# Performance work log

Hardware: AMD Instinct MI355X
Metric: run time of the kernel (lower is better)

The kernel has to match this reference:

```python
import jax, jax.numpy as jnp
import numpy as np

EPS = 1e-08  # attention offset, matches module epsilon


def _ln(x, g, b, eps=1e-5):
    m = jnp.mean(x, axis=-1, keepdims=True)
    v = jnp.var(x, axis=-1, keepdims=True)
    return (x - m) * jax.lax.rsqrt(v + eps) * g + b


def setup_inputs() -> dict:
    key = jax.random.key(0)
    ks = jax.random.split(key, 12)
    B, N, D, S, H = 32, 16384, 64, 7, 128
    sc = 1.0 / np.sqrt(D)
    sch = 1.0 / np.sqrt(H)
    return {
        "inputs": jax.random.normal(ks[0], (B, N, D), jnp.float32),
        "ln_in_g": jnp.ones((D,), jnp.float32), "ln_in_b": jnp.zeros((D,), jnp.float32),
        "ln_slots_g": jnp.ones((D,), jnp.float32), "ln_slots_b": jnp.zeros((D,), jnp.float32),
        "ln_mlp_g": jnp.ones((D,), jnp.float32), "ln_mlp_b": jnp.zeros((D,), jnp.float32),
        "Wq": jax.random.normal(ks[1], (D, D), jnp.float32) * sc,
        "Wk": jax.random.normal(ks[2], (D, D), jnp.float32) * sc,
        "Wv": jax.random.normal(ks[3], (D, D), jnp.float32) * sc,
        "slots_mu": jax.random.normal(ks[4], (1, 1, D), jnp.float32),
        "slots_log_sigma": jax.random.normal(ks[5], (1, 1, D), jnp.float32) * 0.1,
        "w_ih": jax.random.normal(ks[6], (3 * D, D), jnp.float32) * sc,
        "w_hh": jax.random.normal(ks[7], (3 * D, D), jnp.float32) * sc,
        "b_ih": jnp.zeros((3 * D,), jnp.float32), "b_hh": jnp.zeros((3 * D,), jnp.float32),
        "mlp_w1": jax.random.normal(ks[8], (H, D), jnp.float32) * sc,
        "mlp_b1": jnp.zeros((H,), jnp.float32),
        "mlp_w2": jax.random.normal(ks[9], (D, H), jnp.float32) * sch,
        "mlp_b2": jnp.zeros((D,), jnp.float32),
        "noise_slots": jax.random.normal(ks[10], (B, S, D), jnp.float32),
        "noise_h": jax.random.normal(ks[11], (B, D), jnp.float32),
        "num_iterations": 3,
    }


def reference(inputs, ln_in_g, ln_in_b, ln_slots_g, ln_slots_b, ln_mlp_g, ln_mlp_b,
              Wq, Wk, Wv, slots_mu, slots_log_sigma, w_ih, w_hh, b_ih, b_hh,
              mlp_w1, mlp_b1, mlp_w2, mlp_b2, noise_slots, noise_h, num_iterations):
    D = inputs.shape[-1]
    scale = D ** -0.5

    x = _ln(inputs, ln_in_g, ln_in_b)               # [B,N,D]
    k = jnp.einsum('bnd,ed->bne', x, Wk)            # [B,N,D]
    v = jnp.einsum('bnd,ed->bne', x, Wv)            # [B,N,D]

    sigma = jnp.exp(slots_log_sigma)
    slots = slots_mu + sigma * noise_slots          # [B,S,D]
    h0 = (slots_mu + sigma * noise_h[None])[0]      # [B,D] (torch h0 is [1,B,D])

    def gru_step(h, x_t):  # torch GRU cell, gate order r,z,n
        gi = x_t @ w_ih.T + b_ih
        gh = h @ w_hh.T + b_hh
        ir, iz, inn = jnp.split(gi, 3, axis=-1)
        hr, hz, hn = jnp.split(gh, 3, axis=-1)
        r = jax.nn.sigmoid(ir + hr)
        z = jax.nn.sigmoid(iz + hz)
        n = jnp.tanh(inn + r * hn)
        h_new = (1.0 - z) * n + z * h
        return h_new, h_new

    for _ in range(num_iterations):
        sn = _ln(slots, ln_slots_g, ln_slots_b)
        q = jnp.einsum('bsd,ed->bse', sn, Wq) * scale        # [B,S,D]
        logits = jnp.einsum('bnd,bsd->bns', k, q)            # [B,N,S]
        attn = jax.nn.softmax(logits, axis=-1) + EPS          # softmax over slots
        attn = attn / jnp.sum(attn, axis=1, keepdims=True)   # normalize over inputs (dim=-2)
        updates = jnp.einsum('bns,bnd->bsd', attn, v)        # [B,S,D]
        # nn.GRU over the slot axis as "time", fixed h0 each iteration
        _, hs = jax.lax.scan(gru_step, h0, jnp.swapaxes(updates, 0, 1))
        slots = jnp.swapaxes(hs, 0, 1)                       # [B,S,D]
        hid = jax.nn.relu(_ln(slots, ln_mlp_g, ln_mlp_b) @ mlp_w1.T + mlp_b1)
        slots = slots + (hid @ mlp_w2.T + mlp_b2)
    return slots
```

## Files before the change

kernel.cpp:

```cpp
#include <hip/hip_runtime.h>
#include <hip/hip_bf16.h>


#define B_ 32
#define N_ 16384
#define D_ 64
#define S_ 7

typedef __bf16 bf16x8 __attribute__((ext_vector_type(8)));
typedef float floatx4 __attribute__((ext_vector_type(4)));

__device__ __forceinline__ unsigned int f2bfu(float f) {
  __hip_bfloat16 h = __float2bfloat16(f);
  return (unsigned int)__builtin_bit_cast(unsigned short, h);
}
__device__ __forceinline__ unsigned int pack2bf(float lo, float hi) {
  return f2bfu(lo) | (f2bfu(hi) << 16);
}

__global__ __launch_bounds__(256) void proj_kernel(
    const float* __restrict__ x,
    const float* __restrict__ lng, const float* __restrict__ lnb,
    const float* __restrict__ Wk, const float* __restrict__ Wv,
    unsigned short* __restrict__ kt, unsigned short* __restrict__ vb)
{
  __shared__ __align__(16) unsigned short s_xn[128 * 64];
  __shared__ __align__(16) unsigned short s_w[128 * 64];
  const int t = threadIdx.x;
  const int lane = t & 63;
  const int w = t >> 6;
  const int R0 = blockIdx.x * 128;
  const int bb = R0 >> 14;
  const int nbase = R0 & (N_ - 1);

  for (int j = 0; j < 2; ++j) {
    int idx = (t + j * 256) * 16;
    const float* src = (idx < 4096) ? (Wk + idx) : (Wv + idx - 4096);
    float4 a = ((const float4*)src)[0], b = ((const float4*)src)[1];
    float4 c = ((const float4*)src)[2], d = ((const float4*)src)[3];
    uint4 p0, p1;
    p0.x = pack2bf(a.x, a.y); p0.y = pack2bf(a.z, a.w);
    p0.z = pack2bf(b.x, b.y); p0.w = pack2bf(b.z, b.w);
    p1.x = pack2bf(c.x, c.y); p1.y = pack2bf(c.z, c.w);
    p1.z = pack2bf(d.x, d.y); p1.w = pack2bf(d.z, d.w);
    ((uint4*)s_w)[idx >> 3] = p0;
    ((uint4*)s_w)[(idx >> 3) + 1] = p1;
  }

  const int ql = t & 3;
  float4 g4[4], b4[4];
#pragma unroll
  for (int j = 0; j < 4; ++j) {
    g4[j] = *(const float4*)&lng[ql * 16 + j * 4];
    b4[j] = *(const float4*)&lnb[ql * 16 + j * 4];
  }
#pragma unroll
  for (int half = 0; half < 2; ++half) {
    int r = half * 64 + (t >> 2);
    const float4* xp = (const float4*)&x[(size_t)(R0 + r) * 64 + ql * 16];
    float4 xv[4];
#pragma unroll
    for (int j = 0; j < 4; ++j) xv[j] = xp[j];
    float s1 = 0.f, s2 = 0.f;
#pragma unroll
    for (int j = 0; j < 4; ++j) {
      s1 += xv[j].x + xv[j].y + xv[j].z + xv[j].w;
      s2 += xv[j].x * xv[j].x + xv[j].y * xv[j].y + xv[j].z * xv[j].z + xv[j].w * xv[j].w;
    }
    s1 += __shfl_xor(s1, 1); s2 += __shfl_xor(s2, 1);
    s1 += __shfl_xor(s1, 2); s2 += __shfl_xor(s2, 2);
    float mean = s1 * 0.015625f;
    float var = s2 * 0.015625f - mean * mean;
    float rs = rsqrtf(var + 1e-5f);
    float y[16];
#pragma unroll
    for (int j = 0; j < 4; ++j) {
      y[j * 4 + 0] = (xv[j].x - mean) * rs * g4[j].x + b4[j].x;
      y[j * 4 + 1] = (xv[j].y - mean) * rs * g4[j].y + b4[j].y;
      y[j * 4 + 2] = (xv[j].z - mean) * rs * g4[j].z + b4[j].z;
      y[j * 4 + 3] = (xv[j].w - mean) * rs * g4[j].w + b4[j].w;
    }
#pragma unroll
    for (int h = 0; h < 2; ++h) {
      uint4 p;
      p.x = pack2bf(y[h * 8 + 0], y[h * 8 + 1]);
      p.y = pack2bf(y[h * 8 + 2], y[h * 8 + 3]);
      p.z = pack2bf(y[h * 8 + 4], y[h * 8 + 5]);
      p.w = pack2bf(y[h * 8 + 6], y[h * 8 + 7]);
      int c = ql * 2 + h;
      int sc = c ^ (r & 7);
      *(uint4*)&s_xn[r * 64 + sc * 8] = p;
    }
  }
  __syncthreads();

  const int m16 = lane & 15, quad = lane >> 4;
  bf16x8 bf[2][2];
#pragma unroll
  for (int rt = 0; rt < 2; ++rt) {
    int xr = (w * 2 + rt) * 16 + m16;
#pragma unroll
    for (int kt2 = 0; kt2 < 2; ++kt2)
      bf[rt][kt2] = *(const bf16x8*)&s_xn[xr * 64 + (((kt2 * 4 + quad) ^ (xr & 7)) * 8)];
  }

#pragma unroll
  for (int ft = 0; ft < 4; ++ft) {
    bf16x8 wk0 = *(const bf16x8*)&s_w[(ft * 16 + m16) * 64 + quad * 8];
    bf16x8 wk1 = *(const bf16x8*)&s_w[(ft * 16 + m16) * 64 + 32 + quad * 8];
#pragma unroll
    for (int rt = 0; rt < 2; ++rt) {
      floatx4 acc = (floatx4){0.f, 0.f, 0.f, 0.f};
      acc = __builtin_amdgcn_mfma_f32_16x16x32_bf16(bf[rt][0], wk0, acc, 0, 0, 0);
      acc = __builtin_amdgcn_mfma_f32_16x16x32_bf16(bf[rt][1], wk1, acc, 0, 0, 0);
      int n_l = nbase + (w * 2 + rt) * 16 + quad * 4;
      size_t off = ((size_t)bb * 64 + ft * 16 + m16) * N_ + n_l;
      uint2 p;
      p.x = pack2bf(acc[0], acc[1]);
      p.y = pack2bf(acc[2], acc[3]);
      *(uint2*)&kt[off] = p;
    }
  }

#pragma unroll
  for (int mt = 0; mt < 4; ++mt) {
    bf16x8 wv0 = *(const bf16x8*)&s_w[(64 + mt * 16 + m16) * 64 + quad * 8];
    bf16x8 wv1 = *(const bf16x8*)&s_w[(64 + mt * 16 + m16) * 64 + 32 + quad * 8];
#pragma unroll
    for (int nt = 0; nt < 2; ++nt) {
      floatx4 acc = (floatx4){0.f, 0.f, 0.f, 0.f};
      acc = __builtin_amdgcn_mfma_f32_16x16x32_bf16(wv0, bf[nt][0], acc, 0, 0, 0);
      acc = __builtin_amdgcn_mfma_f32_16x16x32_bf16(wv1, bf[nt][1], acc, 0, 0, 0);
      int xrow_g = R0 + (w * 2 + nt) * 16 + m16;
      int col = mt * 16 + quad * 4;
      uint2 p;
      p.x = pack2bf(acc[0], acc[1]);
      p.y = pack2bf(acc[2], acc[3]);
      *(uint2*)&vb[(size_t)xrow_g * 64 + col] = p;
    }
  }
}

__device__ void q_from_slots(const float* s_slot, float* s_tmp,
                             const float* __restrict__ g, const float* __restrict__ bb,
                             const float* __restrict__ Wq, float* __restrict__ qout,
                             int lane, int w)
{
  for (int ss = 0; ss < 2; ++ss) {
    int srow = ss * 4 + w;
    if (srow < 7) {
      float xv = s_slot[srow * 64 + lane];
      float s1 = xv, s2 = xv * xv;
#pragma unroll
      for (int mm = 1; mm < 64; mm <<= 1) {
        s1 += __shfl_xor(s1, mm);
        s2 += __shfl_xor(s2, mm);
      }
      float mean = s1 * 0.015625f;
      float var = s2 * 0.015625f - mean * mean;
      float rs = rsqrtf(var + 1e-5f);
      s_tmp[w * 64 + lane] = (xv - mean) * rs * g[lane] + bb[lane];
    }
    __syncthreads();
    if (srow < 7) {
      float acc = 0.f;
      const float* wr = Wq + lane * 64;
      const float* xr = s_tmp + w * 64;
      for (int d = 0; d < 64; ++d) acc += xr[d] * wr[d];
      qout[srow * 64 + lane] = acc * 0.125f;
    }
    __syncthreads();
  }
}

__global__ __launch_bounds__(256) void init_kernel(
    const float* __restrict__ mu, const float* __restrict__ lsig,
    const float* __restrict__ nslots, const float* __restrict__ nh,
    const float* __restrict__ ln_s_g, const float* __restrict__ ln_s_b,
    const float* __restrict__ Wq,
    float* __restrict__ qbuf, float* __restrict__ Wacc, float* __restrict__ Cacc,
    float* __restrict__ h0b)
{
  __shared__ float s_slot[448];
  __shared__ float s_tmp[256];
  const int b = blockIdx.x, t = threadIdx.x, lane = t & 63, w = t >> 6;
  for (int o = t; o < 448; o += 256) {
    int d = o & 63;
    s_slot[o] = mu[d] + expf(lsig[d]) * nslots[b * 448 + o];
    Wacc[b * 448 + o] = 0.f;
  }
  if (t < 64) h0b[b * 64 + t] = mu[t] + expf(lsig[t]) * nh[b * 64 + t];
  if (t < 8) Cacc[b * 8 + t] = 0.f;
  __syncthreads();
  q_from_slots(s_slot, s_tmp, ln_s_g, ln_s_b, Wq, qbuf + b * 448, lane, w);
}

__global__ __launch_bounds__(256) void attn_kernel(
    const unsigned short* __restrict__ kt, const unsigned short* __restrict__ vb,
    const float* __restrict__ qbuf,
    float* __restrict__ Wacc, float* __restrict__ Cacc)
{
  __shared__ __align__(16) float s_qt[64 * 8];
  __shared__ __align__(16) float s_attn[4][7 * 132];
  __shared__ __align__(16) float s_red[4][448];
  __shared__ float s_cred[4][8];

  const int b = blockIdx.y;
  const int t = threadIdx.x, lane = t & 63, w = t >> 6;

  for (int i = t; i < 448; i += 256) {
    int s = i >> 6, d = i & 63;
    s_qt[d * 8 + s] = qbuf[b * 448 + i];
  }
  if (t < 64) s_qt[t * 8 + 7] = 0.f;
  __syncthreads();

  const int n0 = blockIdx.x * 512 + w * 128;

  float lg[2][7];
#pragma unroll
  for (int j = 0; j < 2; ++j)
#pragma unroll
    for (int s = 0; s < 7; ++s) lg[j][s] = 0.f;

  const unsigned short* ktb = kt + (size_t)b * 64 * N_ + n0 + 2 * lane;
#pragma unroll 16
  for (int d = 0; d < 64; ++d) {
    unsigned int kk = *(const unsigned int*)(ktb + (size_t)d * N_);
    float k0 = __uint_as_float(kk << 16);
    float k1 = __uint_as_float(kk & 0xffff0000u);
    float4 qa = *(const float4*)&s_qt[d * 8];
    float4 qb = *(const float4*)&s_qt[d * 8 + 4];
    lg[0][0] += k0 * qa.x; lg[0][1] += k0 * qa.y; lg[0][2] += k0 * qa.z; lg[0][3] += k0 * qa.w;
    lg[0][4] += k0 * qb.x; lg[0][5] += k0 * qb.y; lg[0][6] += k0 * qb.z;
    lg[1][0] += k1 * qa.x; lg[1][1] += k1 * qa.y; lg[1][2] += k1 * qa.z; lg[1][3] += k1 * qa.w;
    lg[1][4] += k1 * qb.x; lg[1][5] += k1 * qb.y; lg[1][6] += k1 * qb.z;
  }

  float cloc[7];
#pragma unroll
  for (int s = 0; s < 7; ++s) cloc[s] = 0.f;
  float at[2][7];
#pragma unroll
  for (int j = 0; j < 2; ++j) {
    float mx = lg[j][0];
#pragma unroll
    for (int s = 1; s < 7; ++s) mx = fmaxf(mx, lg[j][s]);
    float sum = 0.f;
#pragma unroll
    for (int s = 0; s < 7; ++s) { at[j][s] = __expf(lg[j][s] - mx); sum += at[j][s]; }
    float inv = 1.f / sum;
#pragma unroll
    for (int s = 0; s < 7; ++s) { at[j][s] = at[j][s] * inv + 1e-8f; }
  }
#pragma unroll
  for (int s = 0; s < 7; ++s) {
    cloc[s] = at[0][s] + at[1][s];
    float2 p = {at[0][s], at[1][s]};
    *(float2*)&s_attn[w][s * 132 + 2 * lane] = p;
  }
  asm volatile("s_waitcnt lgkmcnt(0)" ::: "memory");

  const int rq = lane & 3, dq = lane >> 4 ? (lane >> 2) : (lane >> 2);
  float accs[7][4];
#pragma unroll
  for (int s = 0; s < 7; ++s)
#pragma unroll
    for (int j = 0; j < 4; ++j) accs[s][j] = 0.f;

  const unsigned short* vbb = vb + ((size_t)b * N_ + n0) * 64 + (size_t)dq * 4;
#pragma unroll 8
  for (int rr = 0; rr < 32; ++rr) {
    int r = rr * 4 + rq;
    uint2 vv = *(const uint2*)(vbb + (size_t)r * 64);
    float vf0 = __uint_as_float(vv.x << 16);
    float vf1 = __uint_as_float(vv.x & 0xffff0000u);
    float vf2 = __uint_as_float(vv.y << 16);
    float vf3 = __uint_as_float(vv.y & 0xffff0000u);
#pragma unroll
    for (int s = 0; s < 7; ++s) {
      float av = s_attn[w][s * 132 + r];
      accs[s][0] += av * vf0;
      accs[s][1] += av * vf1;
      accs[s][2] += av * vf2;
      accs[s][3] += av * vf3;
    }
  }
#pragma unroll
  for (int s = 0; s < 7; ++s)
#pragma unroll
    for (int j = 0; j < 4; ++j) {
      float v = accs[s][j];
      v += __shfl_xor(v, 1);
      v += __shfl_xor(v, 2);
      accs[s][j] = v;
    }
  if (rq == 0) {
#pragma unroll
    for (int s = 0; s < 7; ++s)
#pragma unroll
      for (int j = 0; j < 4; ++j)
        s_red[w][s * 64 + dq * 4 + j] = accs[s][j];
  }
#pragma unroll
  for (int s = 0; s < 7; ++s) {
    float c = cloc[s];
#pragma unroll
    for (int mm = 1; mm < 64; mm <<= 1) c += __shfl_xor(c, mm);
    cloc[s] = c;
  }
  if (lane == 0) {
#pragma unroll
    for (int s = 0; s < 7; ++s) s_cred[w][s] = cloc[s];
  }
  __syncthreads();
  if (w == 0) {
#pragma unroll
    for (int s = 0; s < 7; ++s) {
      float v = s_red[0][s * 64 + lane] + s_red[1][s * 64 + lane] +
                s_red[2][s * 64 + lane] + s_red[3][s * 64 + lane];
      atomicAdd(&Wacc[b * 448 + s * 64 + lane], v);
    }
    if (lane < 7) {
      float c = s_cred[0][lane] + s_cred[1][lane] + s_cred[2][lane] + s_cred[3][lane];
      atomicAdd(&Cacc[b * 8 + lane], c);
    }
  }
}

__global__ __launch_bounds__(256) void slot_update_kernel(
    float* __restrict__ Wacc, float* __restrict__ Cacc,
    const float* __restrict__ h0b,
    const float* __restrict__ w_ih, const float* __restrict__ w_hh,
    const float* __restrict__ b_ih, const float* __restrict__ b_hh,
    const float* __restrict__ ln_m_g, const float* __restrict__ ln_m_b,
    const float* __restrict__ w1, const float* __restrict__ b1,
    const float* __restrict__ w2, const float* __restrict__ b2,
    const float* __restrict__ ln_s_g, const float* __restrict__ ln_s_b,
    const float* __restrict__ Wq,
    float* __restrict__ qbuf, float* __restrict__ out)
{
  const int b = blockIdx.x, t = threadIdx.x, lane = t & 63, w = t >> 6;
  __shared__ float s_upd[448];
  __shared__ float s_gi[1344];
  __shared__ float s_h[64];
  __shared__ float s_gh[192];
  __shared__ float s_slot[448];
  __shared__ float s_tmp[256];

  for (int o = t; o < 448; o += 256) {
    int s = o >> 6;
    s_upd[o] = Wacc[b * 448 + o] / Cacc[b * 8 + s];
  }
  __syncthreads();
  for (int o = t; o < 1344; o += 256) {
    int s = o / 192, j = o - s * 192;
    float acc = b_ih[j];
    const float* wr = w_ih + j * 64;
    const float* ur = s_upd + s * 64;
    for (int d = 0; d < 64; ++d) acc += ur[d] * wr[d];
    s_gi[o] = acc;
  }
  if (t < 64) s_h[t] = h0b[b * 64 + t];
  __syncthreads();
  for (int s = 0; s < 7; ++s) {
    if (t < 192) {
      float acc = b_hh[t];
      const float* wr = w_hh + t * 64;
      for (int d = 0; d < 64; ++d) acc += s_h[d] * wr[d];
      s_gh[t] = acc;
    }
    __syncthreads();
    if (t < 64) {
      float ir = s_gi[s * 192 + t], iz = s_gi[s * 192 + 64 + t], inn = s_gi[s * 192 + 128 + t];
      float hr = s_gh[t], hz = s_gh[64 + t], hn = s_gh[128 + t];
      float r = 1.f / (1.f + expf(-(ir + hr)));
      float z = 1.f / (1.f + expf(-(iz + hz)));
      float n = tanhf(inn + r * hn);
      float hnew = (1.f - z) * n + z * s_h[t];
      s_slot[s * 64 + t] = hnew;
      s_h[t] = hnew;
    }
    __syncthreads();
  }
  float* s_sn = s_gi;
  float* s_hid = s_gi + 448;
  for (int ss = 0; ss < 2; ++ss) {
    int srow = ss * 4 + w;
    if (srow < 7) {
      float xv = s_slot[srow * 64 + lane];
      float s1 = xv, s2 = xv * xv;
#pragma unroll
      for (int mm = 1; mm < 64; mm <<= 1) {
        s1 += __shfl_xor(s1, mm);
        s2 += __shfl_xor(s2, mm);
      }
      float mean = s1 * 0.015625f;
      float var = s2 * 0.015625f - mean * mean;
      float rs = rsqrtf(var + 1e-5f);
      s_sn[srow * 64 + lane] = (xv - mean) * rs * ln_m_g[lane] + ln_m_b[lane];
    }
  }
  __syncthreads();
  for (int o = t; o < 896; o += 256) {
    int s = o >> 7, hh = o & 127;
    float acc = b1[hh];
    const float* wr = w1 + hh * 64;
    const float* xr = s_sn + s * 64;
    for (int d = 0; d < 64; ++d) acc += xr[d] * wr[d];
    s_hid[o] = fmaxf(acc, 0.f);
  }
  __syncthreads();
  for (int o = t; o < 448; o += 256) {
    int s = o >> 6, d = o & 63;
    float acc = b2[d];
    const float* wr = w2 + d * 128;
    const float* hr = s_hid + s * 128;
    for (int h = 0; h < 128; ++h) acc += hr[h] * wr[h];
    float val = s_slot[o] + acc;
    s_slot[o] = val;
    out[b * 448 + o] = val;
  }
  for (int o = t; o < 448; o += 256) Wacc[b * 448 + o] = 0.f;
  if (t < 8) Cacc[b * 8 + t] = 0.f;
  __syncthreads();
  q_from_slots(s_slot, s_tmp, ln_s_g, ln_s_b, Wq, qbuf + b * 448, lane, w);
}

extern "C" void kernel_launch(void* const* d_in, const int* in_sizes, int n_in,
                              void* d_out, int out_size, void* d_ws, size_t ws_size,
                              hipStream_t stream)
{
  (void)in_sizes; (void)n_in; (void)out_size; (void)ws_size;
  const float* x      = (const float*)d_in[0];
  const float* ln_in_g = (const float*)d_in[1];
  const float* ln_in_b = (const float*)d_in[2];
  const float* ln_s_g  = (const float*)d_in[3];
  const float* ln_s_b  = (const float*)d_in[4];
  const float* ln_m_g  = (const float*)d_in[5];
  const float* ln_m_b  = (const float*)d_in[6];
  const float* Wq = (const float*)d_in[7];
  const float* Wk = (const float*)d_in[8];
  const float* Wv = (const float*)d_in[9];
  const float* mu = (const float*)d_in[10];
  const float* lsig = (const float*)d_in[11];
  const float* w_ih = (const float*)d_in[12];
  const float* w_hh = (const float*)d_in[13];
  const float* b_ih = (const float*)d_in[14];
  const float* b_hh = (const float*)d_in[15];
  const float* w1 = (const float*)d_in[16];
  const float* b1 = (const float*)d_in[17];
  const float* w2 = (const float*)d_in[18];
  const float* b2 = (const float*)d_in[19];
  const float* nslots = (const float*)d_in[20];
  const float* nh = (const float*)d_in[21];

  unsigned short* kt = (unsigned short*)d_ws;
  unsigned short* vb = kt + (size_t)B_ * N_ * D_;
  float* fb = (float*)(vb + (size_t)B_ * N_ * D_);
  float* qbuf = fb;
  float* Wacc = fb + 14336;
  float* Cacc = fb + 28672;
  float* h0b  = fb + 28928;
  float* out = (float*)d_out;

  proj_kernel<<<4096, 256, 0, stream>>>(x, ln_in_g, ln_in_b, Wk, Wv, kt, vb);
  init_kernel<<<32, 256, 0, stream>>>(mu, lsig, nslots, nh, ln_s_g, ln_s_b, Wq,
                                      qbuf, Wacc, Cacc, h0b);
  for (int it = 0; it < 3; ++it) {
    attn_kernel<<<dim3(32, 32), 256, 0, stream>>>(kt, vb, qbuf, Wacc, Cacc);
    slot_update_kernel<<<32, 256, 0, stream>>>(Wacc, Cacc, h0b, w_ih, w_hh, b_ih, b_hh,
                                               ln_m_g, ln_m_b, w1, b1, w2, b2,
                                               ln_s_g, ln_s_b, Wq, qbuf, out);
  }
}
```

Measured before the change: 488.8 us.

## Use MFMA for attention logits and updates with row-major K and transposed V

Swaps the storage layouts: K is now written row-major [B,N,D] and V transposed [B,D,N], each staged through LDS so global stores are coalesced. The attention kernel then computes logits and the attention-weighted V sum with bf16 MFMA instead of scalar FMA loops, doing the slot softmax with lane shuffles. Attention weights are rounded to bf16, which costs some precision. The slot update kernel stages w_hh transposed in LDS for the GRU recurrence, and several small dot products use float4 loads.

After: 423.5 us. -13.4%, faster.

```diff
diff --git a/kernel.cpp b/kernel.cpp
--- a/kernel.cpp
+++ b/kernel.cpp
@@ -22,29 +22,28 @@
     const float* __restrict__ x,
     const float* __restrict__ lng, const float* __restrict__ lnb,
     const float* __restrict__ Wk, const float* __restrict__ Wv,
-    unsigned short* __restrict__ kt, unsigned short* __restrict__ vb)
-{
-  __shared__ __align__(16) unsigned short s_xn[128 * 64];
-  __shared__ __align__(16) unsigned short s_w[128 * 64];
-  const int t = threadIdx.x;
-  const int lane = t & 63;
-  const int w = t >> 6;
+    unsigned short* __restrict__ kb, unsigned short* __restrict__ vt)
+{
+  __shared__ __align__(16) unsigned char smem[32768];
+  unsigned short* s_xn = (unsigned short*)smem;
+  unsigned short* s_w  = (unsigned short*)(smem + 16384);
+  unsigned short* s_ko = (unsigned short*)smem;
+  unsigned short* s_vo = (unsigned short*)smem;
+
+  const int t = threadIdx.x, lane = t & 63, w = t >> 6;
   const int R0 = blockIdx.x * 128;
   const int bb = R0 >> 14;
   const int nbase = R0 & (N_ - 1);
 
-  for (int j = 0; j < 2; ++j) {
-    int idx = (t + j * 256) * 16;
+#pragma unroll
+  for (int p = 0; p < 4; ++p) {
+    int idx = (p * 256 + t) * 8;
     const float* src = (idx < 4096) ? (Wk + idx) : (Wv + idx - 4096);
     float4 a = ((const float4*)src)[0], b = ((const float4*)src)[1];
-    float4 c = ((const float4*)src)[2], d = ((const float4*)src)[3];
-    uint4 p0, p1;
-    p0.x = pack2bf(a.x, a.y); p0.y = pack2bf(a.z, a.w);
-    p0.z = pack2bf(b.x, b.y); p0.w = pack2bf(b.z, b.w);
-    p1.x = pack2bf(c.x, c.y); p1.y = pack2bf(c.z, c.w);
-    p1.z = pack2bf(d.x, d.y); p1.w = pack2bf(d.z, d.w);
-    ((uint4*)s_w)[idx >> 3] = p0;
-    ((uint4*)s_w)[(idx >> 3) + 1] = p1;
+    uint4 pk;
+    pk.x = pack2bf(a.x, a.y); pk.y = pack2bf(a.z, a.w);
+    pk.z = pack2bf(b.x, b.y); pk.w = pack2bf(b.z, b.w);
+    *(uint4*)&s_w[idx] = pk;
   }
 
   const int ql = t & 3;
@@ -100,44 +99,63 @@
   for (int rt = 0; rt < 2; ++rt) {
     int xr = (w * 2 + rt) * 16 + m16;
 #pragma unroll
-    for (int kt2 = 0; kt2 < 2; ++kt2)
-      bf[rt][kt2] = *(const bf16x8*)&s_xn[xr * 64 + (((kt2 * 4 + quad) ^ (xr & 7)) * 8)];
-  }
-
-#pragma unroll
-  for (int ft = 0; ft < 4; ++ft) {
-    bf16x8 wk0 = *(const bf16x8*)&s_w[(ft * 16 + m16) * 64 + quad * 8];
-    bf16x8 wk1 = *(const bf16x8*)&s_w[(ft * 16 + m16) * 64 + 32 + quad * 8];
+    for (int kk = 0; kk < 2; ++kk)
+      bf[rt][kk] = *(const bf16x8*)&s_xn[xr * 64 + (((kk * 4 + quad) ^ (xr & 7)) * 8)];
+  }
+  bf16x8 wkf[4][2], wvf[4][2];
+#pragma unroll
+  for (int ft = 0; ft < 4; ++ft)
+#pragma unroll
+    for (int kk = 0; kk < 2; ++kk) {
+      wkf[ft][kk] = *(const bf16x8*)&s_w[(ft * 16 + m16) * 64 + kk * 32 + quad * 8];
+      wvf[ft][kk] = *(const bf16x8*)&s_w[(64 + ft * 16 + m16) * 64 + kk * 32 + quad * 8];
+    }
+  __syncthreads();
+
+#pragma unroll
+  for (int ft = 0; ft < 4; ++ft)
 #pragma unroll
     for (int rt = 0; rt < 2; ++rt) {
       floatx4 acc = (floatx4){0.f, 0.f, 0.f, 0.f};
-      acc = __builtin_amdgcn_mfma_f32_16x16x32_bf16(bf[rt][0], wk0, acc, 0, 0, 0);
-      acc = __builtin_amdgcn_mfma_f32_16x16x32_bf16(bf[rt][1], wk1, acc, 0, 0, 0);
-      int n_l = nbase + (w * 2 + rt) * 16 + quad * 4;
-      size_t off = ((size_t)bb * 64 + ft * 16 + m16) * N_ + n_l;
+      acc = __builtin_amdgcn_mfma_f32_16x16x32_bf16(wkf[ft][0], bf[rt][0], acc, 0, 0, 0);
+      acc = __builtin_amdgcn_mfma_f32_16x16x32_bf16(wkf[ft][1], bf[rt][1], acc, 0, 0, 0);
+      int n_l = (w * 2 + rt) * 16 + m16;
       uint2 p;
       p.x = pack2bf(acc[0], acc[1]);
       p.y = pack2bf(acc[2], acc[3]);
-      *(uint2*)&kt[off] = p;
-    }
-  }
-
-#pragma unroll
-  for (int mt = 0; mt < 4; ++mt) {
-    bf16x8 wv0 = *(const bf16x8*)&s_w[(64 + mt * 16 + m16) * 64 + quad * 8];
-    bf16x8 wv1 = *(const bf16x8*)&s_w[(64 + mt * 16 + m16) * 64 + 32 + quad * 8];
-#pragma unroll
-    for (int nt = 0; nt < 2; ++nt) {
+      *(uint2*)&s_ko[n_l * 72 + ft * 16 + quad * 4] = p;
+    }
+  __syncthreads();
+#pragma unroll
+  for (int p = 0; p < 4; ++p) {
+    int ii = (p * 256 + t) * 8;
+    int n_l = ii >> 6, dl = ii & 63;
+    uint4 v4 = *(const uint4*)&s_ko[n_l * 72 + dl];
+    *(uint4*)&kb[(size_t)(R0 + n_l) * 64 + dl] = v4;
+  }
+  __syncthreads();
+
+#pragma unroll
+  for (int ft = 0; ft < 4; ++ft)
+#pragma unroll
+    for (int rt = 0; rt < 2; ++rt) {
       floatx4 acc = (floatx4){0.f, 0.f, 0.f, 0.f};
-      acc = __builtin_amdgcn_mfma_f32_16x16x32_bf16(wv0, bf[nt][0], acc, 0, 0, 0);
-      acc = __builtin_amdgcn_mfma_f32_16x16x32_bf16(wv1, bf[nt][1], acc, 0, 0, 0);
-      int xrow_g = R0 + (w * 2 + nt) * 16 + m16;
-      int col = mt * 16 + quad * 4;
+      acc = __builtin_amdgcn_mfma_f32_16x16x32_bf16(bf[rt][0], wvf[ft][0], acc, 0, 0, 0);
+      acc = __builtin_amdgcn_mfma_f32_16x16x32_bf16(bf[rt][1], wvf[ft][1], acc, 0, 0, 0);
+      int n_l = (w * 2 + rt) * 16 + quad * 4;
+      int d0 = ft * 16 + m16;
       uint2 p;
       p.x = pack2bf(acc[0], acc[1]);
       p.y = pack2bf(acc[2], acc[3]);
-      *(uint2*)&vb[(size_t)xrow_g * 64 + col] = p;
-    }
+      *(uint2*)&s_vo[d0 * 136 + n_l] = p;
+    }
+  __syncthreads();
+#pragma unroll
+  for (int p = 0; p < 4; ++p) {
+    int ii = (p * 256 + t) * 8;
+    int d0 = ii >> 7, nl = ii & 127;
+    uint4 v4 = *(const uint4*)&s_vo[d0 * 136 + nl];
+    *(uint4*)&vt[((size_t)bb * 64 + d0) * N_ + nbase + nl] = v4;
   }
 }
 
@@ -164,9 +182,13 @@
     __syncthreads();
     if (srow < 7) {
       float acc = 0.f;
-      const float* wr = Wq + lane * 64;
-      const float* xr = s_tmp + w * 64;
-      for (int d = 0; d < 64; ++d) acc += xr[d] * wr[d];
+      const float4* wr = (const float4*)(Wq + lane * 64);
+      const float4* xr = (const float4*)(s_tmp + w * 64);
+#pragma unroll
+      for (int i = 0; i < 16; ++i) {
+        float4 a = wr[i], xx = xr[i];
+        acc += a.x * xx.x + a.y * xx.y + a.z * xx.z + a.w * xx.w;
+      }
       qout[srow * 64 + lane] = acc * 0.125f;
     }
     __syncthreads();
@@ -196,123 +218,99 @@
 }
 
 __global__ __launch_bounds__(256) void attn_kernel(
-    const unsigned short* __restrict__ kt, const unsigned short* __restrict__ vb,
+    const unsigned short* __restrict__ kb, const unsigned short* __restrict__ vt,
     const float* __restrict__ qbuf,
     float* __restrict__ Wacc, float* __restrict__ Cacc)
 {
-  __shared__ __align__(16) float s_qt[64 * 8];
-  __shared__ __align__(16) float s_attn[4][7 * 132];
+  __shared__ __align__(16) unsigned short s_qb[16 * 64];
+  __shared__ __align__(16) unsigned short s_at[4][16 * 136];
   __shared__ __align__(16) float s_red[4][448];
   __shared__ float s_cred[4][8];
 
   const int b = blockIdx.y;
   const int t = threadIdx.x, lane = t & 63, w = t >> 6;
-
-  for (int i = t; i < 448; i += 256) {
-    int s = i >> 6, d = i & 63;
-    s_qt[d * 8 + s] = qbuf[b * 448 + i];
-  }
-  if (t < 64) s_qt[t * 8 + 7] = 0.f;
-  __syncthreads();
-
-  const int n0 = blockIdx.x * 512 + w * 128;
-
-  float lg[2][7];
-#pragma unroll
-  for (int j = 0; j < 2; ++j)
-#pragma unroll
-    for (int s = 0; s < 7; ++s) lg[j][s] = 0.f;
-
-  const unsigned short* ktb = kt + (size_t)b * 64 * N_ + n0 + 2 * lane;
-#pragma unroll 16
-  for (int d = 0; d < 64; ++d) {
-    unsigned int kk = *(const unsigned int*)(ktb + (size_t)d * N_);
-    float k0 = __uint_as_float(kk << 16);
-    float k1 = __uint_as_float(kk & 0xffff0000u);
-    float4 qa = *(const float4*)&s_qt[d * 8];
-    float4 qb = *(const float4*)&s_qt[d * 8 + 4];
-    lg[0][0] += k0 * qa.x; lg[0][1] += k0 * qa.y; lg[0][2] += k0 * qa.z; lg[0][3] += k0 * qa.w;
-    lg[0][4] += k0 * qb.x; lg[0][5] += k0 * qb.y; lg[0][6] += k0 * qb.z;
-    lg[1][0] += k1 * qa.x; lg[1][1] += k1 * qa.y; lg[1][2] += k1 * qa.z; lg[1][3] += k1 * qa.w;
-    lg[1][4] += k1 * qb.x; lg[1][5] += k1 * qb.y; lg[1][6] += k1 * qb.z;
-  }
-
-  float cloc[7];
-#pragma unroll
-  for (int s = 0; s < 7; ++s) cloc[s] = 0.f;
-  float at[2][7];
-#pragma unroll
-  for (int j = 0; j < 2; ++j) {
-    float mx = lg[j][0];
-#pragma unroll
-    for (int s = 1; s < 7; ++s) mx = fmaxf(mx, lg[j][s]);
-    float sum = 0.f;
-#pragma unroll
-    for (int s = 0; s < 7; ++s) { at[j][s] = __expf(lg[j][s] - mx); sum += at[j][s]; }
-    float inv = 1.f / sum;
-#pragma unroll
-    for (int s = 0; s < 7; ++s) { at[j][s] = at[j][s] * inv + 1e-8f; }
-  }
-#pragma unroll
-  for (int s = 0; s < 7; ++s) {
-    cloc[s] = at[0][s] + at[1][s];
-    float2 p = {at[0][s], at[1][s]};
-    *(float2*)&s_attn[w][s * 132 + 2 * lane] = p;
+  const int m16 = lane & 15, quad = lane >> 4;
+
+  {
+    int i0 = t * 4;
+    int s = i0 >> 6, d0 = i0 & 63;
+    float f0 = 0.f, f1 = 0.f, f2 = 0.f, f3 = 0.f;
+    if (s < 7) {
+      const float* qp = qbuf + b * 448 + s * 64 + d0;
+      f0 = qp[0]; f1 = qp[1]; f2 = qp[2]; f3 = qp[3];
+    }
+    uint2 p;
+    p.x = pack2bf(f0, f1);
+    p.y = pack2bf(f2, f3);
+    *(uint2*)&s_qb[i0] = p;
+  }
+  __syncthreads();
+
+  bf16x8 bq0 = *(const bf16x8*)&s_qb[m16 * 64 + quad * 8];
+  bf16x8 bq1 = *(const bf16x8*)&s_qb[m16 * 64 + 32 + quad * 8];
+
+  const int n0w = blockIdx.x * 512 + w * 128;
+  const unsigned short* kbA = kb + ((size_t)b * N_ + n0w) * 64;
+
+  float cl = 0.f;
+#pragma unroll
+  for (int nt = 0; nt < 8; ++nt) {
+    bf16x8 a0 = *(const bf16x8*)&kbA[(size_t)(nt * 16 + m16) * 64 + quad * 8];
+    bf16x8 a1 = *(const bf16x8*)&kbA[(size_t)(nt * 16 + m16) * 64 + 32 + quad * 8];
+    floatx4 c = (floatx4){0.f, 0.f, 0.f, 0.f};
+    c = __builtin_amdgcn_mfma_f32_16x16x32_bf16(a0, bq0, c, 0, 0, 0);
+    c = __builtin_amdgcn_mfma_f32_16x16x32_bf16(a1, bq1, c, 0, 0, 0);
+    float atv[4];
+#pragma unroll
+    for (int rg = 0; rg < 4; ++rg) {
+      float xx = (m16 < 7) ? c[rg] : -1e30f;
+      float mx = xx;
+      mx = fmaxf(mx, __shfl_xor(mx, 1));
+      mx = fmaxf(mx, __shfl_xor(mx, 2));
+      mx = fmaxf(mx, __shfl_xor(mx, 4));
+      float e = __expf(xx - mx);
+      float sm = e;
+      sm += __shfl_xor(sm, 1);
+      sm += __shfl_xor(sm, 2);
+      sm += __shfl_xor(sm, 4);
+      float a = e / sm + 1e-8f;
+      atv[rg] = a;
+      cl += a;
+    }
+    if (m16 < 7) {
+      uint2 p;
+      p.x = pack2bf(atv[0], atv[1]);
+      p.y = pack2bf(atv[2], atv[3]);
+      *(uint2*)&s_at[w][m16 * 136 + nt * 16 + quad * 4] = p;
+    }
   }
   asm volatile("s_waitcnt lgkmcnt(0)" ::: "memory");
 
-  const int rq = lane & 3, dq = lane >> 4 ? (lane >> 2) : (lane >> 2);
-  float accs[7][4];
-#pragma unroll
-  for (int s = 0; s < 7; ++s)
-#pragma unroll
-    for (int j = 0; j < 4; ++j) accs[s][j] = 0.f;
-
-  const unsigned short* vbb = vb + ((size_t)b * N_ + n0) * 64 + (size_t)dq * 4;
-#pragma unroll 8
-  for (int rr = 0; rr < 32; ++rr) {
-    int r = rr * 4 + rq;
-    uint2 vv = *(const uint2*)(vbb + (size_t)r * 64);
-    float vf0 = __uint_as_float(vv.x << 16);
-    float vf1 = __uint_as_float(vv.x & 0xffff0000u);
-    float vf2 = __uint_as_float(vv.y << 16);
-    float vf3 = __uint_as_float(vv.y & 0xffff0000u);
-#pragma unroll
-    for (int s = 0; s < 7; ++s) {
-      float av = s_attn[w][s * 132 + r];
-      accs[s][0] += av * vf0;
-      accs[s][1] += av * vf1;
-      accs[s][2] += av * vf2;
-      accs[s][3] += av * vf3;
-    }
-  }
-#pragma unroll
-  for (int s = 0; s < 7; ++s)
-#pragma unroll
-    for (int j = 0; j < 4; ++j) {
-      float v = accs[s][j];
-      v += __shfl_xor(v, 1);
-      v += __shfl_xor(v, 2);
-      accs[s][j] = v;
-    }
-  if (rq == 0) {
-#pragma unroll
-    for (int s = 0; s < 7; ++s)
-#pragma unroll
-      for (int j = 0; j < 4; ++j)
-        s_red[w][s * 64 + dq * 4 + j] = accs[s][j];
-  }
-#pragma unroll
-  for (int s = 0; s < 7; ++s) {
-    float c = cloc[s];
-#pragma unroll
-    for (int mm = 1; mm < 64; mm <<= 1) c += __shfl_xor(c, mm);
-    cloc[s] = c;
-  }
-  if (lane == 0) {
-#pragma unroll
-    for (int s = 0; s < 7; ++s) s_cred[w][s] = cloc[s];
-  }
+  floatx4 acc[4];
+#pragma unroll
+  for (int dt = 0; dt < 4; ++dt) acc[dt] = (floatx4){0.f, 0.f, 0.f, 0.f};
+  const unsigned short* vtB = vt + (size_t)b * 64 * N_ + n0w;
+#pragma unroll
+  for (int ch = 0; ch < 4; ++ch) {
+    bf16x8 af = *(const bf16x8*)&s_at[w][m16 * 136 + ch * 32 + quad * 8];
+#pragma unroll
+    for (int dt = 0; dt < 4; ++dt) {
+      bf16x8 bv = *(const bf16x8*)&vtB[(size_t)(dt * 16 + m16) * N_ + ch * 32 + quad * 8];
+      acc[dt] = __builtin_amdgcn_mfma_f32_16x16x32_bf16(af, bv, acc[dt], 0, 0, 0);
+    }
+  }
+  if (quad < 2) {
+#pragma unroll
+    for (int dt = 0; dt < 4; ++dt)
+#pragma unroll
+      for (int rg = 0; rg < 4; ++rg) {
+        int s = quad * 4 + rg;
+        if (s < 7) s_red[w][s * 64 + dt * 16 + m16] = acc[dt][rg];
+      }
+  }
+  cl += __shfl_xor(cl, 16);
+  cl += __shfl_xor(cl, 32);
+  if (m16 < 7 && quad == 0) s_cred[w][m16] = cl;
   __syncthreads();
   if (w == 0) {
 #pragma unroll
@@ -341,6 +339,7 @@
     float* __restrict__ qbuf, float* __restrict__ out)
 {
   const int b = blockIdx.x, t = threadIdx.x, lane = t & 63, w = t >> 6;
+  __shared__ float s_whhT[64 * 201];
   __shared__ float s_upd[448];
   __shared__ float s_gi[1344];
   __shared__ float s_h[64];
@@ -348,26 +347,34 @@
   __shared__ float s_slot[448];
   __shared__ float s_tmp[256];
 
+  for (int i = t; i < 12288; i += 256) {
+    int j = i >> 6, d = i & 63;
+    s_whhT[d * 201 + j] = w_hh[i];
+  }
   for (int o = t; o < 448; o += 256) {
     int s = o >> 6;
     s_upd[o] = Wacc[b * 448 + o] / Cacc[b * 8 + s];
   }
+  if (t < 64) s_h[t] = h0b[b * 64 + t];
   __syncthreads();
   for (int o = t; o < 1344; o += 256) {
     int s = o / 192, j = o - s * 192;
     float acc = b_ih[j];
-    const float* wr = w_ih + j * 64;
-    const float* ur = s_upd + s * 64;
-    for (int d = 0; d < 64; ++d) acc += ur[d] * wr[d];
+    const float4* wr = (const float4*)(w_ih + j * 64);
+    const float4* ur = (const float4*)(s_upd + s * 64);
+#pragma unroll
+    for (int i = 0; i < 16; ++i) {
+      float4 a = wr[i], u = ur[i];
+      acc += a.x * u.x + a.y * u.y + a.z * u.z + a.w * u.w;
+    }
     s_gi[o] = acc;
   }
-  if (t < 64) s_h[t] = h0b[b * 64 + t];
   __syncthreads();
   for (int s = 0; s < 7; ++s) {
     if (t < 192) {
       float acc = b_hh[t];
-      const float* wr = w_hh + t * 64;
-      for (int d = 0; d < 64; ++d) acc += s_h[d] * wr[d];
+#pragma unroll 16
+      for (int d = 0; d < 64; ++d) acc += s_h[d] * s_whhT[d * 201 + t];
       s_gh[t] = acc;
     }
     __syncthreads();
@@ -405,18 +412,26 @@
   for (int o = t; o < 896; o += 256) {
     int s = o >> 7, hh = o & 127;
     float acc = b1[hh];
-    const float* wr = w1 + hh * 64;
-    const float* xr = s_sn + s * 64;
-    for (int d = 0; d < 64; ++d) acc += xr[d] * wr[d];
+    const float4* wr = (const float4*)(w1 + hh * 64);
+    const float4* xr = (const float4*)(s_sn + s * 64);
+#pragma unroll
+    for (int i = 0; i < 16; ++i) {
+      float4 a = wr[i], xx = xr[i];
+      acc += a.x * xx.x + a.y * xx.y + a.z * xx.z + a.w * xx.w;
+    }
     s_hid[o] = fmaxf(acc, 0.f);
   }
   __syncthreads();
   for (int o = t; o < 448; o += 256) {
     int s = o >> 6, d = o & 63;
     float acc = b2[d];
-    const float* wr = w2 + d * 128;
-    const float* hr = s_hid + s * 128;
-    for (int h = 0; h < 128; ++h) acc += hr[h] * wr[h];
+    const float4* wr = (const float4*)(w2 + d * 128);
+    const float4* hr = (const float4*)(s_hid + s * 128);
+#pragma unroll
+    for (int i = 0; i < 32; ++i) {
+      float4 a = wr[i], hv = hr[i];
+      acc += a.x * hv.x + a.y * hv.y + a.z * hv.z + a.w * hv.w;
+    }
     float val = s_slot[o] + acc;
     s_slot[o] = val;
     out[b * 448 + o] = val;
@@ -455,20 +470,20 @@
   const float* nslots = (const float*)d_in[20];
   const float* nh = (const float*)d_in[21];
 
-  unsigned short* kt = (unsigned short*)d_ws;
-  unsigned short* vb = kt + (size_t)B_ * N_ * D_;
-  float* fb = (float*)(vb + (size_t)B_ * N_ * D_);
+  unsigned short* kb = (unsigned short*)d_ws;
+  unsigned short* vt = kb + (size_t)B_ * N_ * D_;
+  float* fb = (float*)(vt + (size_t)B_ * N_ * D_);
   float* qbuf = fb;
   float* Wacc = fb + 14336;
   float* Cacc = fb + 28672;
   float* h0b  = fb + 28928;
   float* out = (float*)d_out;
 
-  proj_kernel<<<4096, 256, 0, stream>>>(x, ln_in_g, ln_in_b, Wk, Wv, kt, vb);
+  proj_kernel<<<4096, 256, 0, stream>>>(x, ln_in_g, ln_in_b, Wk, Wv, kb, vt);
   init_kernel<<<32, 256, 0, stream>>>(mu, lsig, nslots, nh, ln_s_g, ln_s_b, Wq,
                                       qbuf, Wacc, Cacc, h0b);
   for (int it = 0; it < 3; ++it) {
-    attn_kernel<<<dim3(32, 32), 256, 0, stream>>>(kt, vb, qbuf, Wacc, Cacc);
+    attn_kernel<<<dim3(32, 32), 256, 0, stream>>>(kb, vt, qbuf, Wacc, Cacc);
     slot_update_kernel<<<32, 256, 0, stream>>>(Wacc, Cacc, h0b, w_ih, w_hh, b_ih, b_hh,
                                                ln_m_g, ln_m_b, w1, b1, w2, b2,
                                                ln_s_g, ln_s_b, Wq, qbuf, out);
```
